# Kernel tuning notes

Hardware: AMD Instinct MI355X
Metric: run time of the kernel (lower is better)

The kernel has to match this reference:

```python
import jax, jax.numpy as jnp
import numpy as np

B, S = 32, 128
E_NUM, SKILL, D_K, D_E, D_A = 4000, 256, 128, 128, 128
AT_NUM, IT_NUM = 1000, 1000
GAMMA = 0.03


def _lin(key, out_d, in_d):
    # xavier-normal style init
    w = jax.random.normal(key, (out_d, in_d), jnp.float32) * (2.0 / (in_d + out_d)) ** 0.5
    b = jnp.zeros((out_d,), jnp.float32)
    return w, b


def setup_inputs() -> dict:
    key = jax.random.key(0)
    ks = jax.random.split(key, 16)
    exercise_id = jax.random.randint(ks[0], (B, S), 0, E_NUM, jnp.int32)
    ans_time = jax.random.randint(ks[1], (B, S), 0, AT_NUM, jnp.int32)
    interval_time = jax.random.randint(ks[2], (B, S), 0, IT_NUM, jnp.int32)
    answer_value = jax.random.randint(ks[3], (B, S), 0, 2, jnp.int32)
    # enhanced q-matrix: binary with zeros replaced by gamma
    qmask = jax.random.bernoulli(ks[4], 0.1, (E_NUM, SKILL))
    q_matrix = jnp.where(qmask, 1.0, GAMMA).astype(jnp.float32)
    ex_table = jax.random.normal(ks[5], (E_NUM, D_E), jnp.float32)
    at_table = jax.random.normal(ks[6], (AT_NUM, D_K), jnp.float32)
    it_table = jax.random.normal(ks[7], (IT_NUM, D_K), jnp.float32)
    W1, b1 = _lin(ks[8], D_K, D_E + D_K + D_A)   # learning_embed_layer
    Wl, bl = _lin(ks[9], D_K, 4 * D_K)           # learning_layer
    Wg, bg = _lin(ks[10], D_K, 4 * D_K)          # learning_gate
    Wf, bf = _lin(ks[11], D_K, 3 * D_K)          # forgetting_gate
    Wp, bp = _lin(ks[12], D_K, 2 * D_K)          # predicting_layer
    # xavier-uniform initial knowledge state, shared across batch
    lim = (6.0 / (SKILL + D_K)) ** 0.5
    h0 = jax.random.uniform(ks[13], (SKILL, D_K), jnp.float32, -lim, lim)
    return {"exercise_id": exercise_id, "ans_time": ans_time,
            "interval_time": interval_time, "answer_value": answer_value,
            "q_matrix": q_matrix, "ex_table": ex_table, "at_table": at_table,
            "it_table": it_table, "W1": W1, "b1": b1, "Wl": Wl, "bl": bl,
            "Wg": Wg, "bg": bg, "Wf": Wf, "bf": bf, "Wp": Wp, "bp": bp, "h0": h0}


def _forward(exercise_id, ans_time, interval_time, answer_value, q_matrix,
             ex_table, at_table, it_table, W1, b1, Wl, bl, Wg, bg, Wf, bf,
             Wp, bp, h0):
    b, s = exercise_id.shape
    ex = ex_table[exercise_id]                       # (B,S,d_e)
    at = at_table[ans_time]                          # (B,S,d_k)
    it = it_table[interval_time]                     # (B,S,d_k)
    ans = jnp.broadcast_to(answer_value.astype(ex.dtype)[..., None], (b, s, D_A))
    le = jnp.concatenate([ex, at, ans], -1) @ W1.T + b1   # learning embedding (B,S,d_k)
    kv = q_matrix[exercise_id]                       # knowledge vectors (B,S,skill)

    h_pre = jnp.broadcast_to(h0, (b,) + h0.shape)    # (B,skill,d_k)
    h_tilde_pre = jnp.einsum('bs,bsd->bd', kv[:, 0], h_pre)
    learning_pre = jnp.zeros((b, D_K), ex.dtype)

    def step(carry, xs):
        h_pre, h_tilde_pre, learning_pre = carry
        lv, itv, kv_t, kv_next, ex_next = xs
        x4 = jnp.concatenate([learning_pre, itv, lv, h_tilde_pre], -1)
        lg = jnp.tanh(x4 @ Wl.T + bl)
        gate = jax.nn.sigmoid(x4 @ Wg.T + bg)
        LG = gate * (lg + 1.0) * 0.5                 # (B,d_k)
        LG_tilde = kv_t[:, :, None] * LG[:, None, :] # outer product addressing (B,skill,d_k)
        x3 = jnp.concatenate([h_pre,
                              jnp.broadcast_to(LG[:, None, :], h_pre.shape),
                              jnp.broadcast_to(itv[:, None, :], h_pre.shape)], -1)
        f = jax.nn.sigmoid(x3 @ Wf.T + bf)           # forget gate per skill
        h = LG_tilde + f * h_pre                     # updated knowledge state
        h_tilde = jnp.einsum('bs,bsd->bd', kv_next, h)
        pred = jax.nn.sigmoid(jnp.concatenate([ex_next, h_tilde], -1) @ Wp.T + bp)
        return (h, h_tilde, lv), pred

    sw = lambda a: jnp.swapaxes(a, 0, 1)
    xs = (sw(le[:, :-1]), sw(it[:, 1:]), sw(kv[:, :-1]), sw(kv[:, 1:]), sw(ex[:, 1:]))
    _, preds = jax.lax.scan(step, (h_pre, h_tilde_pre, learning_pre), xs)
    return jnp.swapaxes(preds, 0, 1)                 # (B, S-1, d_k)


def reference(exercise_id, ans_time, interval_time, answer_value, q_matrix,
              ex_table, at_table, it_table, W1, b1, Wl, bl, Wg, bg, Wf, bf,
              Wp, bp, h0):
    return _forward(exercise_id, ans_time, interval_time, answer_value, q_matrix,
                    ex_table, at_table, it_table, W1, b1, Wl, bl, Wg, bg, Wf, bf,
                    Wp, bp, h0)
```

## Files before the change

### kernel.cpp

```cpp
#include <hip/hip_runtime.h>

typedef unsigned int u32;
typedef unsigned short u16;
typedef unsigned long long u64;
typedef u16 u16x8 __attribute__((ext_vector_type(8)));
typedef u16 u16x4 __attribute__((ext_vector_type(4)));
typedef __bf16 bf16x8 __attribute__((ext_vector_type(8)));
typedef __bf16 bf16x4v __attribute__((ext_vector_type(4)));
typedef float f32x4 __attribute__((ext_vector_type(4)));
typedef float f32x2 __attribute__((ext_vector_type(2)));

#define B_SZ 32
#define S_SZ 128
#define T_SZ 127
#define DK 128
#define SKILL 256
#define SQTR 64
#define RL 136
#define PP 68
#define NPAIR 8
#define SPIN_CAP (1 << 18)

__device__ __forceinline__ u16x4 cvt4(f32x4 v) {
    return __builtin_bit_cast(u16x4, __builtin_convertvector(v, bf16x4v));
}
__device__ __forceinline__ u16x8 cvt8(f32x4 a, f32x4 b) {
    u16x4 x = cvt4(a), y = cvt4(b);
    u16x8 r;
    r[0]=x[0]; r[1]=x[1]; r[2]=x[2]; r[3]=x[3];
    r[4]=y[0]; r[5]=y[1]; r[6]=y[2]; r[7]=y[3];
    return r;
}
__device__ __forceinline__ u16 bfu(float x) {
    return __builtin_bit_cast(u16, (__bf16)x);
}
__device__ __forceinline__ float sigm(float x) {
    float e = __builtin_amdgcn_exp2f(-1.44269504f * x);
    return __builtin_amdgcn_rcpf(1.f + e);
}
__device__ __forceinline__ float tanh_f(float x) {
    float e = __builtin_amdgcn_exp2f(-2.88539008f * x);
    return 2.f * __builtin_amdgcn_rcpf(1.f + e) - 1.f;
}
__device__ __forceinline__ f32x4 mfma16(u16x8 a, u16x8 bb, f32x4 c) {
    return __builtin_amdgcn_mfma_f32_16x16x32_bf16(
        __builtin_bit_cast(bf16x8, a), __builtin_bit_cast(bf16x8, bb), c, 0, 0, 0);
}
__device__ __forceinline__ float pval(u64 p) {
    return __builtin_bit_cast(float, (u32)p);
}
__device__ __forceinline__ float dot4(f32x4 w, f32x4 x) {
    return w[0] * x[0] + w[1] * x[1] + w[2] * x[2] + w[3] * x[3];
}

__global__ __launch_bounds__(128) void k_le(
    const int* __restrict__ eid, const int* __restrict__ atime,
    const int* __restrict__ ansv, const float* __restrict__ ex_t,
    const float* __restrict__ at_t, const float* __restrict__ W1,
    const float* __restrict__ b1, float* __restrict__ le_ws)
{
    const int o = threadIdx.x;
    const int p0 = blockIdx.x * NPAIR;
    int eP[NPAIR], aP[NPAIR];
    float avP[NPAIR];
    #pragma unroll
    for (int i = 0; i < NPAIR; ++i) {
        int p = p0 + i, b = p / T_SZ, t = p - b * T_SZ;
        int idx = b * S_SZ + t;
        eP[i] = eid[idx];
        aP[i] = atime[idx];
        avP[i] = (float)ansv[idx];
    }
    const float* wr = W1 + o * 384;
    const float bias = b1[o];
    float acc[NPAIR];
    #pragma unroll
    for (int i = 0; i < NPAIR; ++i) acc[i] = bias;
    #pragma unroll 2
    for (int k4 = 0; k4 < 32; ++k4) {
        f32x4 w = *(const f32x4*)(wr + 4 * k4);
        #pragma unroll
        for (int i = 0; i < NPAIR; ++i) {
            f32x4 x = *(const f32x4*)(ex_t + eP[i] * DK + 4 * k4);
            acc[i] += dot4(w, x);
        }
    }
    #pragma unroll 2
    for (int k4 = 32; k4 < 64; ++k4) {
        f32x4 w = *(const f32x4*)(wr + 4 * k4);
        #pragma unroll
        for (int i = 0; i < NPAIR; ++i) {
            f32x4 x = *(const f32x4*)(at_t + aP[i] * DK + 4 * k4 - 128);
            acc[i] += dot4(w, x);
        }
    }
    float wsum = 0.f;
    #pragma unroll 4
    for (int k4 = 64; k4 < 96; ++k4) {
        f32x4 w = *(const f32x4*)(wr + 4 * k4);
        wsum += w[0] + w[1] + w[2] + w[3];
    }
    #pragma unroll
    for (int i = 0; i < NPAIR; ++i)
        le_ws[(p0 + i) * DK + o] = acc[i] + avP[i] * wsum;
}

__global__ __launch_bounds__(128) void k_pre(
    const int* __restrict__ itime, const float* __restrict__ it_t,
    const float* __restrict__ Wl, const float* __restrict__ blv,
    const float* __restrict__ Wg, const float* __restrict__ bgv,
    const float* __restrict__ Wf, const float* __restrict__ bfv,
    const float* __restrict__ le_ws,
    float* __restrict__ PRE_l, float* __restrict__ PRE_g, float* __restrict__ PRE_f)
{
    const int o = threadIdx.x;
    const int p0 = blockIdx.x * NPAIR;
    int ivP[NPAIR], lpOff[NPAIR];
    float mP[NPAIR];
    #pragma unroll
    for (int i = 0; i < NPAIR; ++i) {
        int p = p0 + i, b = p / T_SZ, t = p - b * T_SZ;
        ivP[i] = itime[b * S_SZ + t + 1];
        mP[i] = (t == 0) ? 0.f : 1.f;
        lpOff[i] = ((t == 0) ? p : p - 1) * DK;
    }
    const float* wl = Wl + o * 512;
    const float* wg = Wg + o * 512;
    const float bl0 = blv[o], bg0 = bgv[o];
    float al[NPAIR], ag[NPAIR];
    #pragma unroll
    for (int i = 0; i < NPAIR; ++i) { al[i] = bl0; ag[i] = bg0; }
    #pragma unroll 2
    for (int k4 = 0; k4 < 32; ++k4) {
        f32x4 w  = *(const f32x4*)(wl + 4 * k4);
        f32x4 w2 = *(const f32x4*)(wg + 4 * k4);
        #pragma unroll
        for (int i = 0; i < NPAIR; ++i) {
            f32x4 x = *(const f32x4*)(le_ws + lpOff[i] + 4 * k4);
            #pragma unroll
            for (int j = 0; j < 4; ++j) {
                float xv = x[j] * mP[i];
                al[i] += w[j] * xv;
                ag[i] += w2[j] * xv;
            }
        }
    }
    #pragma unroll 2
    for (int k4 = 0; k4 < 32; ++k4) {
        f32x4 w  = *(const f32x4*)(wl + 128 + 4 * k4);
        f32x4 w2 = *(const f32x4*)(wg + 128 + 4 * k4);
        #pragma unroll
        for (int i = 0; i < NPAIR; ++i) {
            f32x4 x = *(const f32x4*)(it_t + ivP[i] * DK + 4 * k4);
            #pragma unroll
            for (int j = 0; j < 4; ++j) {
                al[i] += w[j] * x[j];
                ag[i] += w2[j] * x[j];
            }
        }
    }
    #pragma unroll 2
    for (int k4 = 0; k4 < 32; ++k4) {
        f32x4 w  = *(const f32x4*)(wl + 256 + 4 * k4);
        f32x4 w2 = *(const f32x4*)(wg + 256 + 4 * k4);
        #pragma unroll
        for (int i = 0; i < NPAIR; ++i) {
            f32x4 x = *(const f32x4*)(le_ws + (p0 + i) * DK + 4 * k4);
            #pragma unroll
            for (int j = 0; j < 4; ++j) {
                al[i] += w[j] * x[j];
                ag[i] += w2[j] * x[j];
            }
        }
    }
    const float bf0 = bfv[o];
    float af[NPAIR];
    #pragma unroll
    for (int i = 0; i < NPAIR; ++i) af[i] = bf0;
    const float* wf = Wf + o * 384 + 256;
    #pragma unroll 2
    for (int k4 = 0; k4 < 32; ++k4) {
        f32x4 w = *(const f32x4*)(wf + 4 * k4);
        #pragma unroll
        for (int i = 0; i < NPAIR; ++i) {
            f32x4 x = *(const f32x4*)(it_t + ivP[i] * DK + 4 * k4);
            af[i] += dot4(w, x);
        }
    }
    #pragma unroll
    for (int i = 0; i < NPAIR; ++i) {
        size_t idx = (size_t)(p0 + i) * DK + o;
        PRE_l[idx] = al[i];
        PRE_g[idx] = ag[i];
        PRE_f[idx] = af[i];
    }
}

__global__ __launch_bounds__(512, 1) void k_main(
    const int* __restrict__ eid, const float* __restrict__ qmat,
    const float* __restrict__ Wl, const float* __restrict__ Wg,
    const float* __restrict__ Wf, const float* __restrict__ h0,
    const float* __restrict__ PRE_l, const float* __restrict__ PRE_g,
    const float* __restrict__ PRE_f, const float* __restrict__ ex_t,
    const float* __restrict__ Wp, const float* __restrict__ bpv,
    float* __restrict__ out, u64* __restrict__ xbuf)
{
    extern __shared__ char smem[];
    u16*   hS   = (u16*)smem;
    float* part = (float*)(smem + 17408);
    u16*   htbf = (u16*)(smem + 52224);
    u16*   LGb  = (u16*)(smem + 52736);
    float* LGf  = (float*)(smem + 53248);
    float* cS   = (float*)(smem + 53760);
    float* htf  = (float*)(smem + 54272);

    const int b    = blockIdx.x;
    const int qid  = blockIdx.y;
    const int tid  = threadIdx.x;
    const int w    = tid >> 6;
    const int lane = tid & 63;
    const int quad = lane >> 4;
    const int l4   = lane & 15;
    const int ih   = w & 1;
    const int jh   = w >> 1;

    u64* xq = xbuf + (size_t)b * 1024;
    const int qa = (qid + 1) & 3, qb2 = (qid + 2) & 3, qc = (qid + 3) & 3;

    const int pj = tid >> 4;
    const int pc = tid & 15;
    f32x4 wp4[4];
    {
        const float* wpr = Wp + (32 * qid + pj) * 256 + pc * 16;
        #pragma unroll
        for (int i = 0; i < 4; ++i) wp4[i] = *(const f32x4*)(wpr + 4 * i);
    }
    const float bp = bpv[32 * qid + pj];

    u16x8 afr[4][4];
    #pragma unroll
    for (int mt = 0; mt < 4; ++mt)
        #pragma unroll
        for (int kt = 0; kt < 4; ++kt) {
            const float* p = Wf + (64 * ih + 16 * mt + l4) * 384 + 32 * kt + quad * 8;
            afr[mt][kt] = cvt8(*(const f32x4*)p, *(const f32x4*)(p + 4));
        }
    u16x8 azf[2][4];
    #pragma unroll
    for (int mt = 0; mt < 2; ++mt)
        #pragma unroll
        for (int kt = 0; kt < 4; ++kt) {
            int d = 16 * w + 8 * mt + (l4 >> 1);
            const float* base = (l4 & 1) ? Wg : Wl;
            const float* p = base + d * 512 + 384 + 32 * kt + quad * 8;
            azf[mt][kt] = cvt8(*(const f32x4*)p, *(const f32x4*)(p + 4));
        }
    u16x8 acf[4];
    #pragma unroll
    for (int kt = 0; kt < 4; ++kt) {
        const float* p = Wf + (16 * w + l4) * 384 + 128 + 32 * kt + quad * 8;
        acf[kt] = cvt8(*(const f32x4*)p, *(const f32x4*)(p + 4));
    }

    const int sl = 16 * jh + l4;
    f32x4 hreg[4];
    #pragma unroll
    for (int mt = 0; mt < 4; ++mt) {
        int d0 = 64 * ih + 16 * mt + quad * 4;
        f32x4 hv = *(const f32x4*)(h0 + (SQTR * qid + sl) * DK + d0);
        hreg[mt] = hv;
        *(u16x4*)(hS + sl * RL + d0) = cvt4(hv);
    }

    float kvt = qmat[eid[b * S_SZ] * SKILL + SQTR * qid + sl];

    f32x4 accF[4];

    {
        float htp[16];
        #pragma unroll
        for (int mt = 0; mt < 4; ++mt)
            #pragma unroll
            for (int r = 0; r < 4; ++r)
                htp[mt * 4 + r] = kvt * hreg[mt][r];
        #pragma unroll
        for (int mt = 0; mt < 4; ++mt)
            #pragma unroll
            for (int r = 0; r < 4; ++r)
                part[(64 * ih + 16 * mt + quad * 4 + r) * PP + jh * 16 + l4] = htp[mt * 4 + r];
        __syncthreads();
        int d = tid >> 2, kq = tid & 3;
        const float* pp = part + d * PP + kq * 16;
        float v = 0.f;
        #pragma unroll
        for (int i4 = 0; i4 < 4; ++i4) {
            f32x4 x = *(const f32x4*)(pp + 4 * i4);
            v += x[0] + x[1] + x[2] + x[3];
        }
        v += __shfl_xor(v, 1, 64);
        v += __shfl_xor(v, 2, 64);
        if (kq == 0) {
            u64 pkt = ((u64)1u << 32) | (u64)__builtin_bit_cast(u32, v);
            __hip_atomic_store(xq + qid * 256 + 128 + d, pkt,
                               __ATOMIC_RELAXED, __HIP_MEMORY_SCOPE_AGENT);
        }
        asm volatile("" ::: "memory");
        #pragma unroll
        for (int mt = 0; mt < 4; ++mt)
            accF[mt] = (f32x4){0.f, 0.f, 0.f, 0.f};
        {
            const u16* bp2 = hS + sl * RL + quad * 8;
            u16x8 bfr[4];
            #pragma unroll
            for (int kt = 0; kt < 4; ++kt) bfr[kt] = *(const u16x8*)(bp2 + kt * 32);
            #pragma unroll
            for (int mt = 0; mt < 4; ++mt)
                #pragma unroll
                for (int kt = 0; kt < 4; ++kt)
                    accF[mt] = mfma16(afr[mt][kt], bfr[kt], accF[mt]);
        }
        if (kq == 0) {
            u64 pa, pb, pc2;
            int spins = 0;
            do {
                pa  = __hip_atomic_load(xq + qa * 256 + 128 + d, __ATOMIC_RELAXED, __HIP_MEMORY_SCOPE_AGENT);
                pb  = __hip_atomic_load(xq + qb2 * 256 + 128 + d, __ATOMIC_RELAXED, __HIP_MEMORY_SCOPE_AGENT);
                pc2 = __hip_atomic_load(xq + qc * 256 + 128 + d, __ATOMIC_RELAXED, __HIP_MEMORY_SCOPE_AGENT);
                if ((u32)(pa >> 32) >= 1u && (u32)(pb >> 32) >= 1u && (u32)(pc2 >> 32) >= 1u) break;
                if (spins > 64) __builtin_amdgcn_s_sleep(1);
            } while (++spins < SPIN_CAP);
            float va = pval(pa), vb = pval(pb), vc = pval(pc2);
            float v0 = (qid == 0) ? v : (qid == 3) ? va : (qid == 2) ? vb : vc;
            float v1 = (qid == 1) ? v : (qid == 0) ? va : (qid == 3) ? vb : vc;
            float v2 = (qid == 2) ? v : (qid == 1) ? va : (qid == 0) ? vb : vc;
            float v3 = (qid == 3) ? v : (qid == 2) ? va : (qid == 1) ? vb : vc;
            float vt = ((v0 + v1) + v2) + v3;
            float hf = (float)(__bf16)vt;
            htbf[d] = bfu(vt);
            htbf[128 + d] = bfu(vt - hf);
        }
        __syncthreads();
    }

    for (int t = 0; t < T_SZ; ++t) {
        const size_t tb = (size_t)(b * T_SZ + t) * DK;

        if (t > 0) {
            int epid = eid[b * S_SZ + t];
            float pacc;
            if (pc < 8) {
                const float* xr = ex_t + epid * DK + pc * 16;
                pacc  = dot4(wp4[0], *(const f32x4*)xr);
                pacc += dot4(wp4[1], *(const f32x4*)(xr + 4));
                pacc += dot4(wp4[2], *(const f32x4*)(xr + 8));
                pacc += dot4(wp4[3], *(const f32x4*)(xr + 12));
            } else {
                const float* xr = htf + (pc - 8) * 16;
                pacc  = dot4(wp4[0], *(const f32x4*)xr);
                pacc += dot4(wp4[1], *(const f32x4*)(xr + 4));
                pacc += dot4(wp4[2], *(const f32x4*)(xr + 8));
                pacc += dot4(wp4[3], *(const f32x4*)(xr + 12));
            }
            pacc += __shfl_xor(pacc, 1, 64);
            pacc += __shfl_xor(pacc, 2, 64);
            pacc += __shfl_xor(pacc, 4, 64);
            pacc += __shfl_xor(pacc, 8, 64);
            if (pc == 0)
                out[(size_t)(b * T_SZ + t - 1) * DK + 32 * qid + pj] = sigm(pacc + bp);
        }

        float kvn = qmat[eid[b * S_SZ + t + 1] * SKILL + SQTR * qid + sl];
        f32x2 pl[2], pg[2];
        #pragma unroll
        for (int mt = 0; mt < 2; ++mt) {
            int d0 = 16 * w + 8 * mt + 2 * quad;
            pl[mt] = *(const f32x2*)(PRE_l + tb + d0);
            pg[mt] = *(const f32x2*)(PRE_g + tb + d0);
        }
        f32x4 pf = *(const f32x4*)(PRE_f + tb + 16 * w + quad * 4);

        f32x4 accZ[2];
        accZ[0] = (f32x4){0.f, 0.f, 0.f, 0.f};
        accZ[1] = (f32x4){0.f, 0.f, 0.f, 0.f};
        #pragma unroll
        for (int kt = 0; kt < 4; ++kt) {
            u16x8 bh = *(const u16x8*)(htbf + 32 * kt + quad * 8);
            u16x8 bl = *(const u16x8*)(htbf + 128 + 32 * kt + quad * 8);
            #pragma unroll
            for (int mt = 0; mt < 2; ++mt) {
                accZ[mt] = mfma16(azf[mt][kt], bh, accZ[mt]);
                accZ[mt] = mfma16(azf[mt][kt], bl, accZ[mt]);
            }
        }
        #pragma unroll
        for (int mt = 0; mt < 2; ++mt) {
            u32 hpack = 0, lpack = 0;
            f32x2 fpack;
            #pragma unroll
            for (int rp = 0; rp < 2; ++rp) {
                float zl = accZ[mt][2 * rp] + pl[mt][rp];
                float zg = accZ[mt][2 * rp + 1] + pg[mt][rp];
                float LGv = sigm(zg) * (tanh_f(zl) + 1.f) * 0.5f;
                float hif = (float)(__bf16)LGv;
                hpack |= ((u32)bfu(LGv)) << (16 * rp);
                lpack |= ((u32)bfu(LGv - hif)) << (16 * rp);
                fpack[rp] = LGv;
            }
            if (l4 == 0) {
                int d0 = 16 * w + 8 * mt + 2 * quad;
                *(u32*)(LGb + d0) = hpack;
                *(u32*)(LGb + 128 + d0) = lpack;
                *(f32x2*)(LGf + d0) = fpack;
            }
        }
        __syncthreads();

        {
            f32x4 accC = (f32x4){0.f, 0.f, 0.f, 0.f};
            #pragma unroll
            for (int kt = 0; kt < 4; ++kt) {
                u16x8 bh = *(const u16x8*)(LGb + 32 * kt + quad * 8);
                u16x8 bl = *(const u16x8*)(LGb + 128 + 32 * kt + quad * 8);
                accC = mfma16(acf[kt], bh, accC);
                accC = mfma16(acf[kt], bl, accC);
            }
            accC += pf;
            if (l4 == 0) *(f32x4*)(cS + 16 * w + quad * 4) = accC;
        }
        __syncthreads();

        float htp[16];
        #pragma unroll
        for (int mt = 0; mt < 4; ++mt) {
            int d0 = 64 * ih + 16 * mt + quad * 4;
            f32x4 lg = *(const f32x4*)(LGf + d0);
            f32x4 cc = *(const f32x4*)(cS + d0);
            f32x4 hv;
            #pragma unroll
            for (int r = 0; r < 4; ++r) {
                float f = sigm(accF[mt][r] + cc[r]);
                float hn = kvt * lg[r] + f * hreg[mt][r];
                hreg[mt][r] = hn;
                htp[mt * 4 + r] = kvn * hn;
                hv[r] = hn;
            }
            *(u16x4*)(hS + sl * RL + d0) = cvt4(hv);
        }
        #pragma unroll
        for (int mt = 0; mt < 4; ++mt)
            #pragma unroll
            for (int r = 0; r < 4; ++r)
                part[(64 * ih + 16 * mt + quad * 4 + r) * PP + jh * 16 + l4] = htp[mt * 4 + r];
        kvt = kvn;
        __syncthreads();

        {
            int d = tid >> 2, kq = tid & 3;
            const float* pp = part + d * PP + kq * 16;
            float v = 0.f;
            #pragma unroll
            for (int i4 = 0; i4 < 4; ++i4) {
                f32x4 x = *(const f32x4*)(pp + 4 * i4);
                v += x[0] + x[1] + x[2] + x[3];
            }
            v += __shfl_xor(v, 1, 64);
            v += __shfl_xor(v, 2, 64);
            const int slot = t & 1;
            const u32 seq = (u32)(t + 2);
            if (kq == 0) {
                u64 pkt = ((u64)seq << 32) | (u64)__builtin_bit_cast(u32, v);
                __hip_atomic_store(xq + qid * 256 + slot * 128 + d, pkt,
                                   __ATOMIC_RELAXED, __HIP_MEMORY_SCOPE_AGENT);
            }
            asm volatile("" ::: "memory");
            #pragma unroll
            for (int mt = 0; mt < 4; ++mt)
                accF[mt] = (f32x4){0.f, 0.f, 0.f, 0.f};
            {
                const u16* bp2 = hS + sl * RL + quad * 8;
                u16x8 bfr[4];
                #pragma unroll
                for (int kt = 0; kt < 4; ++kt) bfr[kt] = *(const u16x8*)(bp2 + kt * 32);
                #pragma unroll
                for (int mt = 0; mt < 4; ++mt)
                    #pragma unroll
                    for (int kt = 0; kt < 4; ++kt)
                        accF[mt] = mfma16(afr[mt][kt], bfr[kt], accF[mt]);
            }
            if (kq == 0) {
                u64 pa, pb, pc2;
                int spins = 0;
                do {
                    pa  = __hip_atomic_load(xq + qa * 256 + slot * 128 + d, __ATOMIC_RELAXED, __HIP_MEMORY_SCOPE_AGENT);
                    pb  = __hip_atomic_load(xq + qb2 * 256 + slot * 128 + d, __ATOMIC_RELAXED, __HIP_MEMORY_SCOPE_AGENT);
                    pc2 = __hip_atomic_load(xq + qc * 256 + slot * 128 + d, __ATOMIC_RELAXED, __HIP_MEMORY_SCOPE_AGENT);
                    if ((u32)(pa >> 32) >= seq && (u32)(pb >> 32) >= seq && (u32)(pc2 >> 32) >= seq) break;
                    if (spins > 64) __builtin_amdgcn_s_sleep(1);
                } while (++spins < SPIN_CAP);
                float va = pval(pa), vb = pval(pb), vc = pval(pc2);
                float v0 = (qid == 0) ? v : (qid == 3) ? va : (qid == 2) ? vb : vc;
                float v1 = (qid == 1) ? v : (qid == 0) ? va : (qid == 3) ? vb : vc;
                float v2 = (qid == 2) ? v : (qid == 1) ? va : (qid == 0) ? vb : vc;
                float v3 = (qid == 3) ? v : (qid == 2) ? va : (qid == 1) ? vb : vc;
                float vt = ((v0 + v1) + v2) + v3;
                float hf = (float)(__bf16)vt;
                htbf[d] = bfu(vt);
                htbf[128 + d] = bfu(vt - hf);
                htf[d] = vt;
            }
        }
        __syncthreads();
    }

    {
        int epid = eid[b * S_SZ + T_SZ];
        float pacc;
        if (pc < 8) {
            const float* xr = ex_t + epid * DK + pc * 16;
            pacc  = dot4(wp4[0], *(const f32x4*)xr);
            pacc += dot4(wp4[1], *(const f32x4*)(xr + 4));
            pacc += dot4(wp4[2], *(const f32x4*)(xr + 8));
            pacc += dot4(wp4[3], *(const f32x4*)(xr + 12));
        } else {
            const float* xr = htf + (pc - 8) * 16;
            pacc  = dot4(wp4[0], *(const f32x4*)xr);
            pacc += dot4(wp4[1], *(const f32x4*)(xr + 4));
            pacc += dot4(wp4[2], *(const f32x4*)(xr + 8));
            pacc += dot4(wp4[3], *(const f32x4*)(xr + 12));
        }
        pacc += __shfl_xor(pacc, 1, 64);
        pacc += __shfl_xor(pacc, 2, 64);
        pacc += __shfl_xor(pacc, 4, 64);
        pacc += __shfl_xor(pacc, 8, 64);
        if (pc == 0)
            out[(size_t)(b * T_SZ + T_SZ - 1) * DK + 32 * qid + pj] = sigm(pacc + bp);
    }
}

extern "C" void kernel_launch(void* const* d_in, const int* in_sizes, int n_in,
                              void* d_out, int out_size, void* d_ws, size_t ws_size,
                              hipStream_t stream) {
    const int* eid     = (const int*)d_in[0];
    const int* atime   = (const int*)d_in[1];
    const int* itime   = (const int*)d_in[2];
    const int* ansv    = (const int*)d_in[3];
    const float* qmat  = (const float*)d_in[4];
    const float* ex_t  = (const float*)d_in[5];
    const float* at_t  = (const float*)d_in[6];
    const float* it_t  = (const float*)d_in[7];
    const float* W1    = (const float*)d_in[8];
    const float* b1    = (const float*)d_in[9];
    const float* Wl    = (const float*)d_in[10];
    const float* blv   = (const float*)d_in[11];
    const float* Wg    = (const float*)d_in[12];
    const float* bgv   = (const float*)d_in[13];
    const float* Wf    = (const float*)d_in[14];
    const float* bfv   = (const float*)d_in[15];
    const float* Wp    = (const float*)d_in[16];
    const float* bpv   = (const float*)d_in[17];
    const float* h0    = (const float*)d_in[18];
    float* out = (float*)d_out;

    const size_t SZ = (size_t)B_SZ * T_SZ * DK;
    float* wsf   = (float*)d_ws;
    float* le_ws = wsf;
    float* PRE_l = wsf + SZ;
    float* PRE_g = wsf + 2 * SZ;
    float* PRE_f = wsf + 3 * SZ;
    u64* xbuf = (u64*)le_ws;

    hipFuncSetAttribute((const void*)k_main,
                        hipFuncAttributeMaxDynamicSharedMemorySize, 86016);

    dim3 gaux(508);
    k_le  <<<gaux, 128, 0, stream>>>(eid, atime, ansv, ex_t, at_t, W1, b1, le_ws);
    k_pre <<<gaux, 128, 0, stream>>>(itime, it_t, Wl, blv, Wg, bgv, Wf, bfv,
                                     le_ws, PRE_l, PRE_g, PRE_f);
    hipMemsetAsync(xbuf, 0, (size_t)B_SZ * 1024 * sizeof(u64), stream);
    k_main<<<dim3(B_SZ, 4), 512, 86016, stream>>>(eid, qmat, Wl, Wg, Wf, h0,
                                                  PRE_l, PRE_g, PRE_f,
                                                  ex_t, Wp, bpv, out, xbuf);
}
```

Baseline: 662.9 us.

## Move prediction layer out of recurrent loop into separate batched kernel

Removes the per-step prediction dot products, shuffles and output writes from the sequential recurrence in k_main. The block with qid 0 now writes each h_tilde to a workspace buffer, and a new k_pred kernel computes all predictions afterwards as a batched matvec over (exercise embedding, h_tilde). This shortens the latency-bound serial critical path at the cost of an extra kernel launch and a global round-trip for h_tilde. Also adds a min-blocks hint to the auxiliary kernels' launch bounds.

New measurement: 599.3 us. 9.6% less time.

```diff
diff --git a/kernel.cpp b/kernel.cpp
--- a/kernel.cpp
+++ b/kernel.cpp
@@ -53,7 +53,7 @@
     return w[0] * x[0] + w[1] * x[1] + w[2] * x[2] + w[3] * x[3];
 }
 
-__global__ __launch_bounds__(128) void k_le(
+__global__ __launch_bounds__(128, 2) void k_le(
     const int* __restrict__ eid, const int* __restrict__ atime,
     const int* __restrict__ ansv, const float* __restrict__ ex_t,
     const float* __restrict__ at_t, const float* __restrict__ W1,
@@ -105,7 +105,7 @@
         le_ws[(p0 + i) * DK + o] = acc[i] + avP[i] * wsum;
 }
 
-__global__ __launch_bounds__(128) void k_pre(
+__global__ __launch_bounds__(128, 2) void k_pre(
     const int* __restrict__ itime, const float* __restrict__ it_t,
     const float* __restrict__ Wl, const float* __restrict__ blv,
     const float* __restrict__ Wg, const float* __restrict__ bgv,
@@ -201,9 +201,8 @@
     const float* __restrict__ Wl, const float* __restrict__ Wg,
     const float* __restrict__ Wf, const float* __restrict__ h0,
     const float* __restrict__ PRE_l, const float* __restrict__ PRE_g,
-    const float* __restrict__ PRE_f, const float* __restrict__ ex_t,
-    const float* __restrict__ Wp, const float* __restrict__ bpv,
-    float* __restrict__ out, u64* __restrict__ xbuf)
+    const float* __restrict__ PRE_f, float* __restrict__ ht_ws,
+    u64* __restrict__ xbuf)
 {
     extern __shared__ char smem[];
     u16*   hS   = (u16*)smem;
@@ -212,7 +211,6 @@
     u16*   LGb  = (u16*)(smem + 52736);
     float* LGf  = (float*)(smem + 53248);
     float* cS   = (float*)(smem + 53760);
-    float* htf  = (float*)(smem + 54272);
 
     const int b    = blockIdx.x;
     const int qid  = blockIdx.y;
@@ -226,16 +224,6 @@
 
     u64* xq = xbuf + (size_t)b * 1024;
     const int qa = (qid + 1) & 3, qb2 = (qid + 2) & 3, qc = (qid + 3) & 3;
-
-    const int pj = tid >> 4;
-    const int pc = tid & 15;
-    f32x4 wp4[4];
-    {
-        const float* wpr = Wp + (32 * qid + pj) * 256 + pc * 16;
-        #pragma unroll
-        for (int i = 0; i < 4; ++i) wp4[i] = *(const f32x4*)(wpr + 4 * i);
-    }
-    const float bp = bpv[32 * qid + pj];
 
     u16x8 afr[4][4];
     #pragma unroll
@@ -344,31 +332,6 @@
 
     for (int t = 0; t < T_SZ; ++t) {
         const size_t tb = (size_t)(b * T_SZ + t) * DK;
-
-        if (t > 0) {
-            int epid = eid[b * S_SZ + t];
-            float pacc;
-            if (pc < 8) {
-                const float* xr = ex_t + epid * DK + pc * 16;
-                pacc  = dot4(wp4[0], *(const f32x4*)xr);
-                pacc += dot4(wp4[1], *(const f32x4*)(xr + 4));
-                pacc += dot4(wp4[2], *(const f32x4*)(xr + 8));
-                pacc += dot4(wp4[3], *(const f32x4*)(xr + 12));
-            } else {
-                const float* xr = htf + (pc - 8) * 16;
-                pacc  = dot4(wp4[0], *(const f32x4*)xr);
-                pacc += dot4(wp4[1], *(const f32x4*)(xr + 4));
-                pacc += dot4(wp4[2], *(const f32x4*)(xr + 8));
-                pacc += dot4(wp4[3], *(const f32x4*)(xr + 12));
-            }
-            pacc += __shfl_xor(pacc, 1, 64);
-            pacc += __shfl_xor(pacc, 2, 64);
-            pacc += __shfl_xor(pacc, 4, 64);
-            pacc += __shfl_xor(pacc, 8, 64);
-            if (pc == 0)
-                out[(size_t)(b * T_SZ + t - 1) * DK + 32 * qid + pj] = sigm(pacc + bp);
-        }
-
         float kvn = qmat[eid[b * S_SZ + t + 1] * SKILL + SQTR * qid + sl];
         f32x2 pl[2], pg[2];
         #pragma unroll
@@ -506,35 +469,52 @@
                 float hf = (float)(__bf16)vt;
                 htbf[d] = bfu(vt);
                 htbf[128 + d] = bfu(vt - hf);
-                htf[d] = vt;
+                if (qid == 0) ht_ws[tb + d] = vt;
             }
         }
         __syncthreads();
     }
-
-    {
-        int epid = eid[b * S_SZ + T_SZ];
-        float pacc;
-        if (pc < 8) {
-            const float* xr = ex_t + epid * DK + pc * 16;
-            pacc  = dot4(wp4[0], *(const f32x4*)xr);
-            pacc += dot4(wp4[1], *(const f32x4*)(xr + 4));
-            pacc += dot4(wp4[2], *(const f32x4*)(xr + 8));
-            pacc += dot4(wp4[3], *(const f32x4*)(xr + 12));
-        } else {
-            const float* xr = htf + (pc - 8) * 16;
-            pacc  = dot4(wp4[0], *(const f32x4*)xr);
-            pacc += dot4(wp4[1], *(const f32x4*)(xr + 4));
-            pacc += dot4(wp4[2], *(const f32x4*)(xr + 8));
-            pacc += dot4(wp4[3], *(const f32x4*)(xr + 12));
-        }
-        pacc += __shfl_xor(pacc, 1, 64);
-        pacc += __shfl_xor(pacc, 2, 64);
-        pacc += __shfl_xor(pacc, 4, 64);
-        pacc += __shfl_xor(pacc, 8, 64);
-        if (pc == 0)
-            out[(size_t)(b * T_SZ + T_SZ - 1) * DK + 32 * qid + pj] = sigm(pacc + bp);
-    }
+}
+
+__global__ __launch_bounds__(128, 2) void k_pred(
+    const int* __restrict__ eid, const float* __restrict__ ex_t,
+    const float* __restrict__ Wp, const float* __restrict__ bpv,
+    const float* __restrict__ ht_ws, float* __restrict__ out)
+{
+    const int o = threadIdx.x;
+    const int p0 = blockIdx.x * NPAIR;
+    int eP[NPAIR];
+    #pragma unroll
+    for (int i = 0; i < NPAIR; ++i) {
+        int p = p0 + i, b = p / T_SZ, t = p - b * T_SZ;
+        eP[i] = eid[b * S_SZ + t + 1];
+    }
+    const float* wr = Wp + o * 256;
+    const float bias = bpv[o];
+    float acc[NPAIR];
+    #pragma unroll
+    for (int i = 0; i < NPAIR; ++i) acc[i] = bias;
+    #pragma unroll 2
+    for (int k4 = 0; k4 < 32; ++k4) {
+        f32x4 w = *(const f32x4*)(wr + 4 * k4);
+        #pragma unroll
+        for (int i = 0; i < NPAIR; ++i) {
+            f32x4 x = *(const f32x4*)(ex_t + eP[i] * DK + 4 * k4);
+            acc[i] += dot4(w, x);
+        }
+    }
+    #pragma unroll 2
+    for (int k4 = 32; k4 < 64; ++k4) {
+        f32x4 w = *(const f32x4*)(wr + 4 * k4);
+        #pragma unroll
+        for (int i = 0; i < NPAIR; ++i) {
+            f32x4 x = *(const f32x4*)(ht_ws + (size_t)(p0 + i) * DK + 4 * k4 - 128);
+            acc[i] += dot4(w, x);
+        }
+    }
+    #pragma unroll
+    for (int i = 0; i < NPAIR; ++i)
+        out[(size_t)(p0 + i) * DK + o] = sigm(acc[i]);
 }
 
 extern "C" void kernel_launch(void* const* d_in, const int* in_sizes, int n_in,
@@ -567,6 +547,7 @@
     float* PRE_l = wsf + SZ;
     float* PRE_g = wsf + 2 * SZ;
     float* PRE_f = wsf + 3 * SZ;
+    float* ht_ws = wsf + 4 * SZ;
     u64* xbuf = (u64*)le_ws;
 
     hipFuncSetAttribute((const void*)k_main,
@@ -578,6 +559,7 @@
                                      le_ws, PRE_l, PRE_g, PRE_f);
     hipMemsetAsync(xbuf, 0, (size_t)B_SZ * 1024 * sizeof(u64), stream);
     k_main<<<dim3(B_SZ, 4), 512, 86016, stream>>>(eid, qmat, Wl, Wg, Wf, h0,
-                                                  PRE_l, PRE_g, PRE_f,
-                                                  ex_t, Wp, bpv, out, xbuf);
-}
+                                                  PRE_l, PRE_g, PRE_f, ht_ws,
+                                                  xbuf);
+    k_pred<<<gaux, 128, 0, stream>>>(eid, ex_t, Wp, bpv, ht_ws, out);
+}
```
